# Performance work log

Hardware: AMD Instinct MI355X
Metric: run time of the kernel (lower is better)

Reference implementation:

```python
import jax, jax.numpy as jnp
import numpy as np

N_NODES = 100000
N_EDGES = 1600000
IN_CH = 64
OUT_CH = 64
EDGE_DIM = 32


def setup_inputs() -> dict:
    key = jax.random.key(0)
    ks = jax.random.split(key, 8)
    cat_dim = 2 * IN_CH + EDGE_DIM  # 160
    x = jax.random.normal(ks[0], (N_NODES, IN_CH), dtype=jnp.float32)
    edge_index = jax.random.randint(ks[1], (2, N_EDGES), 0, N_NODES, dtype=jnp.int64)
    edge_attr = jax.random.normal(ks[2], (N_EDGES, EDGE_DIM), dtype=jnp.float32)
    # linear1: (2*in + edge_dim) -> out ; stored as [in, out] for x @ W
    W1 = jax.random.normal(ks[3], (cat_dim, OUT_CH), dtype=jnp.float32) / np.sqrt(cat_dim)
    b1 = jnp.zeros((OUT_CH,), dtype=jnp.float32)
    gamma = jnp.ones((OUT_CH,), dtype=jnp.float32)
    beta = jnp.zeros((OUT_CH,), dtype=jnp.float32)
    W2 = jax.random.normal(ks[4], (OUT_CH, OUT_CH), dtype=jnp.float32) / np.sqrt(OUT_CH)
    b2 = jnp.zeros((OUT_CH,), dtype=jnp.float32)
    return {"x": x, "edge_index": edge_index, "edge_attr": edge_attr,
            "W1": W1, "b1": b1, "gamma": gamma, "beta": beta, "W2": W2, "b2": b2}


def _layer_norm(h, gamma, beta, eps=1e-5):
    mu = jnp.mean(h, axis=-1, keepdims=True)
    var = jnp.var(h, axis=-1, keepdims=True)
    return (h - mu) * jax.lax.rsqrt(var + eps) * gamma + beta


def reference(x, edge_index, edge_attr, W1, b1, gamma, beta, W2, b2):
    i, j = edge_index[0], edge_index[1]
    # gather source/target node features and concat with edge features: [E, 2*in+edge_dim]
    feats = jnp.concatenate([x[i], x[j], edge_attr], axis=-1)
    h = feats @ W1 + b1                       # [E, out]
    h = jax.nn.gelu(_layer_norm(h, gamma, beta), approximate=False)
    m = h @ W2 + b2                           # [E, out]
    # scatter-add messages onto target nodes j, dim_size = N
    return jax.ops.segment_sum(m, j, num_segments=x.shape[0])
```

## Files before the change

### kernel.cpp

```cpp
#include <hip/hip_runtime.h>
#include <math.h>


using short8 = __attribute__((ext_vector_type(8))) short;
using f32x4  = __attribute__((ext_vector_type(4))) float;

#define LDH 72

static __device__ __forceinline__ short f2bf(float f) {
    unsigned u = __float_as_uint(f);
    u += 0x7FFFu + ((u >> 16) & 1u);
    return (short)(u >> 16);
}

static __device__ __forceinline__ short8 pack8(float4 a, float4 b) {
    short8 r;
    r[0] = f2bf(a.x); r[1] = f2bf(a.y); r[2] = f2bf(a.z); r[3] = f2bf(a.w);
    r[4] = f2bf(b.x); r[5] = f2bf(b.y); r[6] = f2bf(b.z); r[7] = f2bf(b.w);
    return r;
}

__global__ void prep_weights(const float* __restrict__ W1,
                             const float* __restrict__ W2,
                             short* __restrict__ Wt1,
                             short* __restrict__ Wt2)
{
    int t = blockIdx.x * blockDim.x + threadIdx.x;
    if (t < 160 * 64) {
        int k = t / 64, n = t % 64;
        Wt1[n * 160 + k] = f2bf(W1[t]);
    }
    int t2 = t - 160 * 64;
    if (t2 >= 0 && t2 < 64 * 64) {
        int k = t2 / 64, n = t2 % 64;
        Wt2[n * 64 + k] = f2bf(W2[t2]);
    }
}

__global__ __launch_bounds__(256) void mpconv_mfma(
    const float* __restrict__ x,
    const int*   __restrict__ ei,
    const float* __restrict__ ea,
    const short* __restrict__ Wt1,
    const float* __restrict__ b1,
    const float* __restrict__ gam,
    const float* __restrict__ bet,
    const short* __restrict__ Wt2,
    const float* __restrict__ b2,
    float*       __restrict__ out,
    int E)
{
    __shared__ __align__(16) short Hlds[4][64][LDH];

    const int wave = threadIdx.x >> 6;
    const int lane = threadIdx.x & 63;
    const int g    = lane >> 4;
    const int col  = lane & 15;
    const int eb   = blockIdx.x * 256 + wave * 64;

    int aedge[4], ii[4], jj[4];
#pragma unroll
    for (int mt = 0; mt < 4; mt++) {
        int e = eb + mt * 16 + col;
        e = (e < E) ? e : (E - 1);
        aedge[mt] = e;
        ii[mt] = ei[e];
        jj[mt] = ei[E + e];
    }

    float b1c[4], gc[4], bc[4], b2c[4];
#pragma unroll
    for (int nt = 0; nt < 4; nt++) {
        int c = col + 16 * nt;
        b1c[nt] = b1[c]; gc[nt] = gam[c]; bc[nt] = bet[c]; b2c[nt] = b2[c];
    }

    f32x4 acc[4][4];
#pragma unroll
    for (int mt = 0; mt < 4; mt++)
#pragma unroll
        for (int nt = 0; nt < 4; nt++)
            acc[mt][nt] = (f32x4){0.f, 0.f, 0.f, 0.f};

#pragma unroll
    for (int ks = 0; ks < 5; ks++) {
        const int k0 = ks * 32;
        const int kk = k0 + g * 8;

        short8 afrag[4];
#pragma unroll
        for (int mt = 0; mt < 4; mt++) {
            const float* s;
            if (k0 < 64)       s = x  + (size_t)ii[mt] * 64 + kk;
            else if (k0 < 128) s = x  + (size_t)jj[mt] * 64 + (kk - 64);
            else               s = ea + (size_t)aedge[mt] * 32 + (kk - 128);
            float4 a = *(const float4*)s;
            float4 b = *(const float4*)(s + 4);
            afrag[mt] = pack8(a, b);
        }
        short8 bfrag[4];
#pragma unroll
        for (int nt = 0; nt < 4; nt++)
            bfrag[nt] = *(const short8*)(Wt1 + (size_t)(col + 16 * nt) * 160 + kk);

#pragma unroll
        for (int mt = 0; mt < 4; mt++)
#pragma unroll
            for (int nt = 0; nt < 4; nt++)
                acc[mt][nt] = __builtin_amdgcn_mfma_f32_16x16x32_bf16(
                    afrag[mt], bfrag[nt], acc[mt][nt], 0, 0, 0);
    }

#pragma unroll
    for (int mt = 0; mt < 4; mt++) {
        float s[4] = {0.f, 0.f, 0.f, 0.f};
        float q[4] = {0.f, 0.f, 0.f, 0.f};
#pragma unroll
        for (int nt = 0; nt < 4; nt++) {
#pragma unroll
            for (int r = 0; r < 4; r++) {
                float v = acc[mt][nt][r] + b1c[nt];
                acc[mt][nt][r] = v;
                s[r] += v;
                q[r] += v * v;
            }
        }
#pragma unroll
        for (int m = 1; m < 16; m <<= 1) {
#pragma unroll
            for (int r = 0; r < 4; r++) {
                s[r] += __shfl_xor(s[r], m);
                q[r] += __shfl_xor(q[r], m);
            }
        }
#pragma unroll
        for (int r = 0; r < 4; r++) {
            float mu  = s[r] * (1.0f / 64.0f);
            float var = q[r] * (1.0f / 64.0f) - mu * mu;
            float inv = rsqrtf(var + 1e-5f);
            int row = mt * 16 + g * 4 + r;
#pragma unroll
            for (int nt = 0; nt < 4; nt++) {
                float h = (acc[mt][nt][r] - mu) * inv * gc[nt] + bc[nt];
                h = 0.5f * h * (1.0f + erff(h * 0.70710678118654752f));
                Hlds[wave][row][col + 16 * nt] = f2bf(h);
            }
        }
    }
    __syncthreads();

    f32x4 acc2[4][4];
#pragma unroll
    for (int mt = 0; mt < 4; mt++)
#pragma unroll
        for (int nt = 0; nt < 4; nt++)
            acc2[mt][nt] = (f32x4){0.f, 0.f, 0.f, 0.f};

#pragma unroll
    for (int ks = 0; ks < 2; ks++) {
        const int kk = ks * 32 + g * 8;
        short8 af[4], bf[4];
#pragma unroll
        for (int mt = 0; mt < 4; mt++)
            af[mt] = *(const short8*)&Hlds[wave][mt * 16 + col][kk];
#pragma unroll
        for (int nt = 0; nt < 4; nt++)
            bf[nt] = *(const short8*)(Wt2 + (size_t)(col + 16 * nt) * 64 + kk);
#pragma unroll
        for (int mt = 0; mt < 4; mt++)
#pragma unroll
            for (int nt = 0; nt < 4; nt++)
                acc2[mt][nt] = __builtin_amdgcn_mfma_f32_16x16x32_bf16(
                    af[mt], bf[nt], acc2[mt][nt], 0, 0, 0);
    }

#pragma unroll
    for (int mt = 0; mt < 4; mt++) {
#pragma unroll
        for (int r = 0; r < 4; r++) {
            int e = eb + mt * 16 + g * 4 + r;
            if (e < E) {
                int dst = ei[E + e];
                float* op = out + (size_t)dst * 64 + col;
#pragma unroll
                for (int nt = 0; nt < 4; nt++)
                    unsafeAtomicAdd(op + 16 * nt, acc2[mt][nt][r] + b2c[nt]);
            }
        }
    }
}

extern "C" void kernel_launch(void* const* d_in, const int* in_sizes, int n_in,
                              void* d_out, int out_size, void* d_ws, size_t ws_size,
                              hipStream_t stream)
{
    const float* x   = (const float*)d_in[0];
    const int*   ei  = (const int*)  d_in[1];
    const float* ea  = (const float*)d_in[2];
    const float* W1  = (const float*)d_in[3];
    const float* b1  = (const float*)d_in[4];
    const float* gam = (const float*)d_in[5];
    const float* bet = (const float*)d_in[6];
    const float* W2  = (const float*)d_in[7];
    const float* b2  = (const float*)d_in[8];
    float* out = (float*)d_out;

    const int E = in_sizes[1] / 2;

    short* Wt1 = (short*)d_ws;
    short* Wt2 = Wt1 + 160 * 64;

    hipMemsetAsync(d_out, 0, (size_t)out_size * sizeof(float), stream);

    {
        int total = 160 * 64 + 64 * 64;
        int grid = (total + 255) / 256;
        hipLaunchKernelGGL(prep_weights, dim3(grid), dim3(256), 0, stream,
                           W1, W2, Wt1, Wt2);
    }
    {
        int grid = (E + 255) / 256;
        hipLaunchKernelGGL(mpconv_mfma, dim3(grid), dim3(256), 0, stream,
                           x, ei, ea, Wt1, b1, gam, bet, Wt2, b2, out, E);
    }
}
```

Before: 760.3 us.

## Precompute per-node W1 projections and move W2 GEMM after scatter

Exploits linearity twice. First, x@W1a and x@W1b are computed once per node and stored as bf16, so each edge gathers 128 bf16 values instead of 128 fp32 raw features. Second, the W2 GEMM is moved after the segment sum, applied per node on the aggregated GELU outputs, with the bias scaled by the node's degree. This removes the per-edge second GEMM and its LDS staging, at the cost of extra kernels, workspace buffers, an additional degree atomic and bf16 rounding of intermediate projections. The edge GEMM keeps a K=160 loop using identity weight blocks, which spends MFMA work on the identity portion.

```diff
diff --git a/kernel.cpp b/kernel.cpp
--- a/kernel.cpp
+++ b/kernel.cpp
@@ -4,8 +4,6 @@
 
 using short8 = __attribute__((ext_vector_type(8))) short;
 using f32x4  = __attribute__((ext_vector_type(4))) float;
-
-#define LDH 72
 
 static __device__ __forceinline__ short f2bf(float f) {
     unsigned u = __float_as_uint(f);
@@ -20,43 +18,103 @@
     return r;
 }
 
-__global__ void prep_weights(const float* __restrict__ W1,
-                             const float* __restrict__ W2,
-                             short* __restrict__ Wt1,
-                             short* __restrict__ Wt2)
+__global__ void prep_weights2(const float* __restrict__ W1,
+                              const float* __restrict__ W2,
+                              short* __restrict__ WtExt,
+                              short* __restrict__ Wab,
+                              short* __restrict__ Wt2t)
 {
     int t = blockIdx.x * blockDim.x + threadIdx.x;
-    if (t < 160 * 64) {
-        int k = t / 64, n = t % 64;
-        Wt1[n * 160 + k] = f2bf(W1[t]);
-    }
-    int t2 = t - 160 * 64;
-    if (t2 >= 0 && t2 < 64 * 64) {
-        int k = t2 / 64, n = t2 % 64;
-        Wt2[n * 64 + k] = f2bf(W2[t2]);
-    }
-}
-
-__global__ __launch_bounds__(256) void mpconv_mfma(
-    const float* __restrict__ x,
+    if (t < 64 * 160) {
+        int n = t / 160, k = t % 160;
+        float v;
+        if (k < 64)       v = (k == n) ? 1.0f : 0.0f;
+        else if (k < 128) v = ((k - 64) == n) ? 1.0f : 0.0f;
+        else              v = W1[(size_t)k * 64 + n];
+        WtExt[t] = f2bf(v);
+    } else if (t < 64 * 160 + 128 * 64) {
+        int t2 = t - 64 * 160;
+        int n = t2 / 64, k = t2 % 64;
+        float v = (n < 64) ? W1[(size_t)k * 64 + n]
+                           : W1[(size_t)(64 + k) * 64 + (n - 64)];
+        Wab[t2] = f2bf(v);
+    } else if (t < 64 * 160 + 128 * 64 + 64 * 64) {
+        int t3 = t - 64 * 160 - 128 * 64;
+        int n = t3 / 64, k = t3 % 64;
+        Wt2t[t3] = f2bf(W2[(size_t)k * 64 + n]);
+    }
+}
+
+__global__ __launch_bounds__(256) void precompute_xab(
+    const float* __restrict__ x, const short* __restrict__ Wab,
+    short* __restrict__ xab, int N)
+{
+    const int wave = threadIdx.x >> 6, lane = threadIdx.x & 63;
+    const int g = lane >> 4, col = lane & 15;
+    const int base = blockIdx.x * 256 + wave * 64;
+
+    short8 af[4][2];
+#pragma unroll
+    for (int mt = 0; mt < 4; mt++) {
+        int row = base + mt * 16 + col;
+        row = (row < N) ? row : (N - 1);
+#pragma unroll
+        for (int ks = 0; ks < 2; ks++) {
+            const float* s = x + (size_t)row * 64 + ks * 32 + g * 8;
+            af[mt][ks] = pack8(*(const float4*)s, *(const float4*)(s + 4));
+        }
+    }
+#pragma unroll
+    for (int half = 0; half < 2; half++) {
+        f32x4 acc[4][4];
+#pragma unroll
+        for (int mt = 0; mt < 4; mt++)
+#pragma unroll
+            for (int nt = 0; nt < 4; nt++)
+                acc[mt][nt] = (f32x4){0.f, 0.f, 0.f, 0.f};
+#pragma unroll
+        for (int ks = 0; ks < 2; ks++) {
+            short8 bf[4];
+#pragma unroll
+            for (int nt = 0; nt < 4; nt++)
+                bf[nt] = *(const short8*)(Wab +
+                    (size_t)(half * 64 + col + 16 * nt) * 64 + ks * 32 + g * 8);
+#pragma unroll
+            for (int mt = 0; mt < 4; mt++)
+#pragma unroll
+                for (int nt = 0; nt < 4; nt++)
+                    acc[mt][nt] = __builtin_amdgcn_mfma_f32_16x16x32_bf16(
+                        af[mt][ks], bf[nt], acc[mt][nt], 0, 0, 0);
+        }
+#pragma unroll
+        for (int mt = 0; mt < 4; mt++)
+#pragma unroll
+            for (int r = 0; r < 4; r++) {
+                int node = base + mt * 16 + g * 4 + r;
+                if (node < N)
+#pragma unroll
+                    for (int nt = 0; nt < 4; nt++)
+                        xab[(size_t)node * 128 + half * 64 + col + 16 * nt] =
+                            f2bf(acc[mt][nt][r]);
+            }
+    }
+}
+
+__global__ __launch_bounds__(256) void mpconv_edge2(
+    const short* __restrict__ xab,
     const int*   __restrict__ ei,
     const float* __restrict__ ea,
-    const short* __restrict__ Wt1,
+    const short* __restrict__ WtExt,
     const float* __restrict__ b1,
     const float* __restrict__ gam,
     const float* __restrict__ bet,
-    const short* __restrict__ Wt2,
-    const float* __restrict__ b2,
-    float*       __restrict__ out,
+    float*       __restrict__ Hsum,
+    float*       __restrict__ deg,
     int E)
 {
-    __shared__ __align__(16) short Hlds[4][64][LDH];
-
-    const int wave = threadIdx.x >> 6;
-    const int lane = threadIdx.x & 63;
-    const int g    = lane >> 4;
-    const int col  = lane & 15;
-    const int eb   = blockIdx.x * 256 + wave * 64;
+    const int wave = threadIdx.x >> 6, lane = threadIdx.x & 63;
+    const int g = lane >> 4, col = lane & 15;
+    const int eb = blockIdx.x * 256 + wave * 64;
 
     int aedge[4], ii[4], jj[4];
 #pragma unroll
@@ -68,11 +126,11 @@
         jj[mt] = ei[E + e];
     }
 
-    float b1c[4], gc[4], bc[4], b2c[4];
+    float b1c[4], gc[4], bc[4];
 #pragma unroll
     for (int nt = 0; nt < 4; nt++) {
         int c = col + 16 * nt;
-        b1c[nt] = b1[c]; gc[nt] = gam[c]; bc[nt] = bet[c]; b2c[nt] = b2[c];
+        b1c[nt] = b1[c]; gc[nt] = gam[c]; bc[nt] = bet[c];
     }
 
     f32x4 acc[4][4];
@@ -83,32 +141,41 @@
             acc[mt][nt] = (f32x4){0.f, 0.f, 0.f, 0.f};
 
 #pragma unroll
-    for (int ks = 0; ks < 5; ks++) {
-        const int k0 = ks * 32;
-        const int kk = k0 + g * 8;
-
-        short8 afrag[4];
+    for (int ks = 0; ks < 4; ks++) {
+        const int kk = ks * 32 + g * 8;
+        short8 af[4], bf[4];
 #pragma unroll
         for (int mt = 0; mt < 4; mt++) {
-            const float* s;
-            if (k0 < 64)       s = x  + (size_t)ii[mt] * 64 + kk;
-            else if (k0 < 128) s = x  + (size_t)jj[mt] * 64 + (kk - 64);
-            else               s = ea + (size_t)aedge[mt] * 32 + (kk - 128);
-            float4 a = *(const float4*)s;
-            float4 b = *(const float4*)(s + 4);
-            afrag[mt] = pack8(a, b);
-        }
-        short8 bfrag[4];
-#pragma unroll
-        for (int nt = 0; nt < 4; nt++)
-            bfrag[nt] = *(const short8*)(Wt1 + (size_t)(col + 16 * nt) * 160 + kk);
-
+            int node = (ks < 2) ? ii[mt] : jj[mt];
+            af[mt] = *(const short8*)(xab + (size_t)node * 128 + kk);
+        }
+#pragma unroll
+        for (int nt = 0; nt < 4; nt++)
+            bf[nt] = *(const short8*)(WtExt + (size_t)(col + 16 * nt) * 160 + kk);
 #pragma unroll
         for (int mt = 0; mt < 4; mt++)
 #pragma unroll
             for (int nt = 0; nt < 4; nt++)
                 acc[mt][nt] = __builtin_amdgcn_mfma_f32_16x16x32_bf16(
-                    afrag[mt], bfrag[nt], acc[mt][nt], 0, 0, 0);
+                    af[mt], bf[nt], acc[mt][nt], 0, 0, 0);
+    }
+    {
+        const int kk = 128 + g * 8;
+        short8 af[4], bf[4];
+#pragma unroll
+        for (int mt = 0; mt < 4; mt++) {
+            const float* s = ea + (size_t)aedge[mt] * 32 + (kk - 128);
+            af[mt] = pack8(*(const float4*)s, *(const float4*)(s + 4));
+        }
+#pragma unroll
+        for (int nt = 0; nt < 4; nt++)
+            bf[nt] = *(const short8*)(WtExt + (size_t)(col + 16 * nt) * 160 + kk);
+#pragma unroll
+        for (int mt = 0; mt < 4; mt++)
+#pragma unroll
+            for (int nt = 0; nt < 4; nt++)
+                acc[mt][nt] = __builtin_amdgcn_mfma_f32_16x16x32_bf16(
+                    af[mt], bf[nt], acc[mt][nt], 0, 0, 0);
     }
 
 #pragma unroll
@@ -116,7 +183,7 @@
         float s[4] = {0.f, 0.f, 0.f, 0.f};
         float q[4] = {0.f, 0.f, 0.f, 0.f};
 #pragma unroll
-        for (int nt = 0; nt < 4; nt++) {
+        for (int nt = 0; nt < 4; nt++)
 #pragma unroll
             for (int r = 0; r < 4; r++) {
                 float v = acc[mt][nt][r] + b1c[nt];
@@ -124,70 +191,98 @@
                 s[r] += v;
                 q[r] += v * v;
             }
-        }
-#pragma unroll
-        for (int m = 1; m < 16; m <<= 1) {
+#pragma unroll
+        for (int m = 1; m < 16; m <<= 1)
 #pragma unroll
             for (int r = 0; r < 4; r++) {
                 s[r] += __shfl_xor(s[r], m);
                 q[r] += __shfl_xor(q[r], m);
             }
-        }
 #pragma unroll
         for (int r = 0; r < 4; r++) {
             float mu  = s[r] * (1.0f / 64.0f);
             float var = q[r] * (1.0f / 64.0f) - mu * mu;
             float inv = rsqrtf(var + 1e-5f);
-            int row = mt * 16 + g * 4 + r;
 #pragma unroll
             for (int nt = 0; nt < 4; nt++) {
                 float h = (acc[mt][nt][r] - mu) * inv * gc[nt] + bc[nt];
-                h = 0.5f * h * (1.0f + erff(h * 0.70710678118654752f));
-                Hlds[wave][row][col + 16 * nt] = f2bf(h);
-            }
-        }
-    }
-    __syncthreads();
-
-    f32x4 acc2[4][4];
+                acc[mt][nt][r] =
+                    0.5f * h * (1.0f + erff(h * 0.70710678118654752f));
+            }
+        }
+    }
+
 #pragma unroll
     for (int mt = 0; mt < 4; mt++)
-#pragma unroll
-        for (int nt = 0; nt < 4; nt++)
-            acc2[mt][nt] = (f32x4){0.f, 0.f, 0.f, 0.f};
-
-#pragma unroll
-    for (int ks = 0; ks < 2; ks++) {
-        const int kk = ks * 32 + g * 8;
-        short8 af[4], bf[4];
-#pragma unroll
-        for (int mt = 0; mt < 4; mt++)
-            af[mt] = *(const short8*)&Hlds[wave][mt * 16 + col][kk];
-#pragma unroll
-        for (int nt = 0; nt < 4; nt++)
-            bf[nt] = *(const short8*)(Wt2 + (size_t)(col + 16 * nt) * 64 + kk);
-#pragma unroll
-        for (int mt = 0; mt < 4; mt++)
-#pragma unroll
-            for (int nt = 0; nt < 4; nt++)
-                acc2[mt][nt] = __builtin_amdgcn_mfma_f32_16x16x32_bf16(
-                    af[mt], bf[nt], acc2[mt][nt], 0, 0, 0);
-    }
-
-#pragma unroll
-    for (int mt = 0; mt < 4; mt++) {
 #pragma unroll
         for (int r = 0; r < 4; r++) {
             int e = eb + mt * 16 + g * 4 + r;
             if (e < E) {
                 int dst = ei[E + e];
-                float* op = out + (size_t)dst * 64 + col;
+                float* hp = Hsum + (size_t)dst * 64 + col;
 #pragma unroll
                 for (int nt = 0; nt < 4; nt++)
-                    unsafeAtomicAdd(op + 16 * nt, acc2[mt][nt][r] + b2c[nt]);
-            }
-        }
-    }
+                    unsafeAtomicAdd(hp + 16 * nt, acc[mt][nt][r]);
+                if (col == 0) unsafeAtomicAdd(deg + dst, 1.0f);
+            }
+        }
+}
+
+__global__ __launch_bounds__(256) void final_node(
+    const float* __restrict__ Hsum, const float* __restrict__ deg,
+    const short* __restrict__ Wt2t, const float* __restrict__ b2,
+    float* __restrict__ out, int N)
+{
+    const int wave = threadIdx.x >> 6, lane = threadIdx.x & 63;
+    const int g = lane >> 4, col = lane & 15;
+    const int base = blockIdx.x * 256 + wave * 64;
+
+    float b2c[4];
+#pragma unroll
+    for (int nt = 0; nt < 4; nt++) b2c[nt] = b2[col + 16 * nt];
+
+    f32x4 acc[4][4];
+#pragma unroll
+    for (int mt = 0; mt < 4; mt++)
+#pragma unroll
+        for (int nt = 0; nt < 4; nt++)
+            acc[mt][nt] = (f32x4){0.f, 0.f, 0.f, 0.f};
+
+#pragma unroll
+    for (int ks = 0; ks < 2; ks++) {
+        const int kk = ks * 32 + g * 8;
+        short8 af[4], bf[4];
+#pragma unroll
+        for (int mt = 0; mt < 4; mt++) {
+            int row = base + mt * 16 + col;
+            row = (row < N) ? row : (N - 1);
+            const float* s = Hsum + (size_t)row * 64 + kk;
+            af[mt] = pack8(*(const float4*)s, *(const float4*)(s + 4));
+        }
+#pragma unroll
+        for (int nt = 0; nt < 4; nt++)
+            bf[nt] = *(const short8*)(Wt2t + (size_t)(col + 16 * nt) * 64 + kk);
+#pragma unroll
+        for (int mt = 0; mt < 4; mt++)
+#pragma unroll
+            for (int nt = 0; nt < 4; nt++)
+                acc[mt][nt] = __builtin_amdgcn_mfma_f32_16x16x32_bf16(
+                    af[mt], bf[nt], acc[mt][nt], 0, 0, 0);
+    }
+
+#pragma unroll
+    for (int mt = 0; mt < 4; mt++)
+#pragma unroll
+        for (int r = 0; r < 4; r++) {
+            int node = base + mt * 16 + g * 4 + r;
+            if (node < N) {
+                float d = deg[node];
+#pragma unroll
+                for (int nt = 0; nt < 4; nt++)
+                    out[(size_t)node * 64 + col + 16 * nt] =
+                        acc[mt][nt][r] + d * b2c[nt];
+            }
+        }
 }
 
 extern "C" void kernel_launch(void* const* d_in, const int* in_sizes, int n_in,
@@ -206,21 +301,29 @@
     float* out = (float*)d_out;
 
     const int E = in_sizes[1] / 2;
-
-    short* Wt1 = (short*)d_ws;
-    short* Wt2 = Wt1 + 160 * 64;
-
-    hipMemsetAsync(d_out, 0, (size_t)out_size * sizeof(float), stream);
+    const int N = in_sizes[0] / 64;
+
+    char* ws = (char*)d_ws;
+    short* WtExt = (short*)(ws);
+    short* Wt2t  = (short*)(ws + 20480);
+    short* Wab   = (short*)(ws + 28672);
+    short* xab   = (short*)(ws + 45056);
+    float* Hsum  = (float*)(ws + 45056 + (size_t)N * 256);
+    float* deg   = (float*)(ws + 45056 + (size_t)N * 256 + (size_t)N * 256);
+
+    hipMemsetAsync(Hsum, 0, (size_t)N * 64 * sizeof(float), stream);
+    hipMemsetAsync(deg, 0, (size_t)N * sizeof(float), stream);
 
     {
-        int total = 160 * 64 + 64 * 64;
-        int grid = (total + 255) / 256;
-        hipLaunchKernelGGL(prep_weights, dim3(grid), dim3(256), 0, stream,
-                           W1, W2, Wt1, Wt2);
-    }
-    {
-        int grid = (E + 255) / 256;
-        hipLaunchKernelGGL(mpconv_mfma, dim3(grid), dim3(256), 0, stream,
-                           x, ei, ea, Wt1, b1, gam, bet, Wt2, b2, out, E);
-    }
-}
+        int total = 64 * 160 + 128 * 64 + 64 * 64;
+        hipLaunchKernelGGL(prep_weights2, dim3((total + 255) / 256), dim3(256),
+                           0, stream, W1, W2, WtExt, Wab, Wt2t);
+    }
+    hipLaunchKernelGGL(precompute_xab, dim3((N + 255) / 256), dim3(256),
+                       0, stream, x, Wab, xab, N);
+    hipLaunchKernelGGL(mpconv_edge2, dim3((E + 255) / 256), dim3(256),
+                       0, stream, xab, ei, ea, WtExt, b1, gam, bet,
+                       Hsum, deg, E);
+    hipLaunchKernelGGL(final_node, dim3((N + 255) / 256), dim3(256),
+                       0, stream, Hsum, deg, Wt2t, b2, out, N);
+}
```

Result: slower. 963.8 us (+26.8%).
